# Kernel optimization log

Measured on AMD Instinct MI355X. Metric: run time of the kernel, lower is better.

Reference implementation:

```python
import jax, jax.numpy as jnp
import numpy as np

B, L, S, H, E = 2, 2048, 2048, 8, 64

def setup_inputs() -> dict:
    key = jax.random.key(0)
    k1, k2, k3 = jax.random.split(key, 3)
    queries = jax.random.normal(k1, (B, L, H, E), dtype=jnp.float32)
    keys = jax.random.normal(k2, (B, S, H, E), dtype=jnp.float32)
    values = jax.random.normal(k3, (B, S, H, E), dtype=jnp.float32)
    # TriangularCausalMask: True above the diagonal (positions to mask out)
    attn_mask = jnp.broadcast_to(
        jnp.triu(jnp.ones((L, S), dtype=bool), k=1)[None, None], (B, 1, L, S)
    )
    return {"queries": queries, "keys": keys, "values": values, "attn_mask": attn_mask}

def reference(queries, keys, values, attn_mask):
    E_ = queries.shape[-1]
    scale = 1.0 / (E_ ** 0.5)  # self.scale is None -> 1/sqrt(E)
    # scores: [B, H, L, S]
    scores = jnp.einsum('blhe,bshe->bhls', queries, keys)
    scores = jnp.where(attn_mask, -jnp.inf, scores)  # masked_fill_(mask, -inf)
    series = jax.nn.softmax(scale * scores, axis=-1)  # dropout p=0.0 -> identity
    V = jnp.einsum('bhls,bshd->blhd', series, values)
    return V, series
```

## Files before the change

### kernel.cpp

```cpp
#include <hip/hip_runtime.h>
#include <hip/hip_bf16.h>

typedef __attribute__((ext_vector_type(8))) short bf16x8;
typedef __attribute__((ext_vector_type(4))) short s16x4;
typedef __attribute__((ext_vector_type(4))) float f32x4;

constexpr int B = 2, L = 2048, S = 2048, H = 8, E = 64;
constexpr int TL = 64;
constexpr int SN = 64;
constexpr int LDK = 72;
constexpr int THREADS = 256;
constexpr int GSTR = H * E;

__device__ __forceinline__ short f2bf(float x) {
  union { float f; unsigned u; } c; c.f = x;
  unsigned r = c.u + 0x7fffu + ((c.u >> 16) & 1u);
  return (short)(r >> 16);
}
__device__ __forceinline__ float bf2f(short s) {
  union { unsigned u; float f; } c; c.u = ((unsigned)(unsigned short)s) << 16;
  return c.f;
}
__device__ __forceinline__ f32x4 mk4(float a, float b, float c, float d) {
  f32x4 v; v[0] = a; v[1] = b; v[2] = c; v[3] = d; return v;
}

struct Tile16 { f32x4 v0, v1, v2, v3; };

__device__ __forceinline__ void ld_tile(const float* __restrict__ g, int tid, Tile16& t) {
  const int r = tid >> 2, c = (tid & 3) * 16;
  const f32x4* q = (const f32x4*)(g + (size_t)r * GSTR + c);
  t.v0 = q[0]; t.v1 = q[1]; t.v2 = q[2]; t.v3 = q[3];
}

__device__ __forceinline__ void cvt_tile(const Tile16& t, short* __restrict__ o) {
  float vv[16] = { t.v0[0],t.v0[1],t.v0[2],t.v0[3], t.v1[0],t.v1[1],t.v1[2],t.v1[3],
                   t.v2[0],t.v2[1],t.v2[2],t.v2[3], t.v3[0],t.v3[1],t.v3[2],t.v3[3] };
#pragma unroll
  for (int k = 0; k < 8; ++k) {
    __hip_bfloat162 h = __float22bfloat162_rn(make_float2(vv[2*k], vv[2*k+1]));
    short2 s2 = *(short2*)&h;
    o[2*k] = s2.x; o[2*k+1] = s2.y;
  }
}

__device__ __forceinline__ void stK(const Tile16& t, short (* __restrict__ Kb)[LDK], int tid) {
  const int r = tid >> 2, c = (tid & 3) * 16;
  short s[16]; cvt_tile(t, s);
  *(bf16x8*)&Kb[r][c]     = *(bf16x8*)&s[0];
  *(bf16x8*)&Kb[r][c + 8] = *(bf16x8*)&s[8];
}

__device__ __forceinline__ void stV(const Tile16& t, short (* __restrict__ Vb)[LDK], int tid) {
  const int sr = tid >> 2, c = (tid & 3) * 16;
  short s[16]; cvt_tile(t, s);
#pragma unroll
  for (int i = 0; i < 16; ++i) {
    const int e = c + i;
    Vb[e][sr ^ (8 * ((e >> 3) & 7))] = s[i];
  }
}

__global__ __launch_bounds__(THREADS, 2)
void attn_tile(const float* __restrict__ Q, const float* __restrict__ K,
               const float* __restrict__ V, float* __restrict__ outV,
               float* __restrict__ outS)
{
  __shared__ __align__(16) short Qs[TL][LDK];
  __shared__ __align__(16) short Ks[2][SN][LDK];
  __shared__ __align__(16) short Vt[2][E][LDK];
  __shared__ __align__(16) short Ps[4][16][LDK];
  __shared__ float inv_lds[TL];

  const int tid  = threadIdx.x;
  const int lane = tid & 63;
  const int wv   = tid >> 6;
  const int quad = lane >> 4;
  const int n16  = lane & 15;

  int t = blockIdx.x;
  t = (t & 1) ? (31 - (t >> 1)) : (t >> 1);
  const int bh = blockIdx.y;
  const int b = bh >> 3, h = bh & 7;
  const int l0 = t * TL;
  const int s_hi = l0 + TL;
  const int nt = s_hi / SN;

  const size_t qbase = ((size_t)b * L * H + h) * E;
  const size_t kbase = ((size_t)b * S * H + h) * E;
  const size_t srow  = (size_t)bh * L * S;

  {
    const f32x4 z = {0.f, 0.f, 0.f, 0.f};
    for (int r = 0; r < TL; ++r) {
      f32x4* p = (f32x4*)(outS + srow + (size_t)(l0 + r) * S);
      for (int s4 = s_hi / 4 + tid; s4 < S / 4; s4 += THREADS)
        __builtin_nontemporal_store(z, p + s4);
    }
  }

  Tile16 pk;
  ld_tile(K + kbase, tid, pk);
  {
    Tile16 tq;
    ld_tile(Q + qbase + (size_t)l0 * GSTR, tid, tq);
    stK(tq, Qs, tid);
  }
  __syncthreads();

  bf16x8 a0 = *(const bf16x8*)&Qs[wv * 16 + n16][quad * 8];
  bf16x8 a1 = *(const bf16x8*)&Qs[wv * 16 + n16][32 + quad * 8];

  float rsum[4] = {0.f, 0.f, 0.f, 0.f};
  for (int st = 0; st < nt; ++st) {
    short (*Kb)[LDK] = Ks[st & 1];
    stK(pk, Kb, tid);
    if (st + 1 < nt)
      ld_tile(K + kbase + (size_t)(st + 1) * SN * GSTR, tid, pk);
    __syncthreads();

    const int s0 = st * SN;
#pragma unroll
    for (int nn = 0; nn < 4; ++nn) {
      bf16x8 b0 = *(const bf16x8*)&Kb[nn * 16 + n16][quad * 8];
      bf16x8 b1 = *(const bf16x8*)&Kb[nn * 16 + n16][32 + quad * 8];
      f32x4 acc = {0.f, 0.f, 0.f, 0.f};
      acc = __builtin_amdgcn_mfma_f32_16x16x32_bf16(a0, b0, acc, 0, 0, 0);
      acc = __builtin_amdgcn_mfma_f32_16x16x32_bf16(a1, b1, acc, 0, 0, 0);
#pragma unroll
      for (int r = 0; r < 4; ++r) {
        const int l = l0 + wv * 16 + quad * 4 + r;
        const int s = s0 + nn * 16 + n16;
        rsum[r] += (s <= l) ? __expf(acc[r] * 0.125f) : 0.f;
      }
    }
  }

  Tile16 pk2, pv2;
  ld_tile(K + kbase, tid, pk2);
  ld_tile(V + kbase, tid, pv2);

#pragma unroll
  for (int r = 0; r < 4; ++r)
#pragma unroll
    for (int off = 1; off < 16; off <<= 1)
      rsum[r] += __shfl_xor(rsum[r], off, 64);
  if (n16 == 0)
#pragma unroll
    for (int r = 0; r < 4; ++r)
      inv_lds[wv * 16 + quad * 4 + r] = 1.f / rsum[r];
  __syncthreads();

  float inv_r[4];
#pragma unroll
  for (int r = 0; r < 4; ++r) inv_r[r] = inv_lds[wv * 16 + quad * 4 + r];

  f32x4 oacc[4] = {{0,0,0,0},{0,0,0,0},{0,0,0,0},{0,0,0,0}};
  for (int st = 0; st < nt; ++st) {
    const int s0 = st * SN;
    short (*Kb)[LDK] = Ks[st & 1];
    short (*Vb)[LDK] = Vt[st & 1];
    stK(pk2, Kb, tid);
    stV(pv2, Vb, tid);
    if (st + 1 < nt) {
      ld_tile(K + kbase + (size_t)(st + 1) * SN * GSTR, tid, pk2);
      ld_tile(V + kbase + (size_t)(st + 1) * SN * GSTR, tid, pv2);
    }
    __syncthreads();

#pragma unroll
    for (int nn = 0; nn < 4; ++nn) {
      bf16x8 b0 = *(const bf16x8*)&Kb[nn * 16 + n16][quad * 8];
      bf16x8 b1 = *(const bf16x8*)&Kb[nn * 16 + n16][32 + quad * 8];
      f32x4 acc = {0.f, 0.f, 0.f, 0.f};
      acc = __builtin_amdgcn_mfma_f32_16x16x32_bf16(a0, b0, acc, 0, 0, 0);
      acc = __builtin_amdgcn_mfma_f32_16x16x32_bf16(a1, b1, acc, 0, 0, 0);
#pragma unroll
      for (int r = 0; r < 4; ++r) {
        const int l = l0 + wv * 16 + quad * 4 + r;
        const int s = s0 + nn * 16 + n16;
        float w = (s <= l) ? __expf(acc[r] * 0.125f) * inv_r[r] : 0.f;
        Ps[wv][quad * 4 + r][(nn * 16 + n16) ^ (8 * quad)] = f2bf(w);
      }
    }

    asm volatile("s_waitcnt lgkmcnt(0)" ::: "memory");

    {
      const int row = lane >> 2;
      const int sub = lane & 3;
      const int swz = 8 * (lane >> 4);
      float* dstrow = outS + srow + (size_t)(l0 + wv * 16 + row) * S + s0;
#pragma unroll
      for (int i = 0; i < 4; ++i) {
        const int c = (i * 16 + sub * 4) ^ swz;
        s16x4 pw = *(const s16x4*)&Ps[wv][row][c];
        f32x4 o = mk4(bf2f(pw[0]), bf2f(pw[1]), bf2f(pw[2]), bf2f(pw[3]));
        __builtin_nontemporal_store(o, (f32x4*)(dstrow + i * 16 + sub * 4));
      }
    }

    {
      const int psw = 8 * ((n16 >> 2) & 3);
      bf16x8 pa0 = *(const bf16x8*)&Ps[wv][n16][(quad * 8)      ^ psw];
      bf16x8 pa1 = *(const bf16x8*)&Ps[wv][n16][(32 + quad * 8) ^ psw];
#pragma unroll
      for (int nn = 0; nn < 4; ++nn) {
        const int e   = nn * 16 + n16;
        const int vsw = 8 * ((e >> 3) & 7);
        bf16x8 vb0 = *(const bf16x8*)&Vb[e][(quad * 8)      ^ vsw];
        bf16x8 vb1 = *(const bf16x8*)&Vb[e][(32 + quad * 8) ^ vsw];
        oacc[nn] = __builtin_amdgcn_mfma_f32_16x16x32_bf16(pa0, vb0, oacc[nn], 0, 0, 0);
        oacc[nn] = __builtin_amdgcn_mfma_f32_16x16x32_bf16(pa1, vb1, oacc[nn], 0, 0, 0);
      }
    }
  }

#pragma unroll
  for (int nn = 0; nn < 4; ++nn)
#pragma unroll
    for (int r = 0; r < 4; ++r) {
      const int l = l0 + wv * 16 + quad * 4 + r;
      __builtin_nontemporal_store(oacc[nn][r],
          &outV[qbase + (size_t)l * GSTR + nn * 16 + n16]);
    }
}

extern "C" void kernel_launch(void* const* d_in, const int* in_sizes, int n_in,
                              void* d_out, int out_size, void* d_ws, size_t ws_size,
                              hipStream_t stream) {
  const float* Q = (const float*)d_in[0];
  const float* K = (const float*)d_in[1];
  const float* V = (const float*)d_in[2];
  float* outV = (float*)d_out;
  float* outS = outV + (size_t)B * L * H * E;
  attn_tile<<<dim3(L / TL, B * H), THREADS, 0, stream>>>(Q, K, V, outV, outS);
}
```

Measured before the change: 408.4 us.

## Split attention into row-sum kernel and split-S PV kernel with atomics

Splits the single fused kernel into two launches. The first computes softmax denominators, zero-fills the masked score region and zeroes the output, writing inverse row sums to the workspace. The second splits each query tile's key range into two halves across separate blocks, accumulating output with atomicAdd. The aim is to give the heavy PV/score-write phase more parallelism and better load balance, at the cost of an extra launch, a global round-trip for the row sums, recomputed Q conversion, and atomic traffic.

After: 388.1 us. 1.05x faster.

```diff
diff --git a/kernel.cpp b/kernel.cpp
--- a/kernel.cpp
+++ b/kernel.cpp
@@ -12,14 +12,14 @@
 constexpr int THREADS = 256;
 constexpr int GSTR = H * E;
 
+__device__ __forceinline__ float bf2f(short s) {
+  union { unsigned u; float f; } c; c.u = ((unsigned)(unsigned short)s) << 16;
+  return c.f;
+}
 __device__ __forceinline__ short f2bf(float x) {
   union { float f; unsigned u; } c; c.f = x;
   unsigned r = c.u + 0x7fffu + ((c.u >> 16) & 1u);
   return (short)(r >> 16);
-}
-__device__ __forceinline__ float bf2f(short s) {
-  union { unsigned u; float f; } c; c.u = ((unsigned)(unsigned short)s) << 16;
-  return c.f;
 }
 __device__ __forceinline__ f32x4 mk4(float a, float b, float c, float d) {
   f32x4 v; v[0] = a; v[1] = b; v[2] = c; v[3] = d; return v;
@@ -61,16 +61,29 @@
   }
 }
 
+__device__ __forceinline__ bf16x8 cvt8(f32x4 u0, f32x4 u1) {
+  short o[8];
+  float vv[8] = { u0[0],u0[1],u0[2],u0[3], u1[0],u1[1],u1[2],u1[3] };
+#pragma unroll
+  for (int k = 0; k < 4; ++k) {
+    __hip_bfloat162 h = __float22bfloat162_rn(make_float2(vv[2*k], vv[2*k+1]));
+    short2 s2 = *(short2*)&h;
+    o[2*k] = s2.x; o[2*k+1] = s2.y;
+  }
+  return *(bf16x8*)o;
+}
+
+__device__ __forceinline__ int swz_t(int raw) {
+  return (raw & 1) ? (31 - (raw >> 1)) : (raw >> 1);
+}
+
 __global__ __launch_bounds__(THREADS, 2)
-void attn_tile(const float* __restrict__ Q, const float* __restrict__ K,
-               const float* __restrict__ V, float* __restrict__ outV,
-               float* __restrict__ outS)
+void k_rowsum(const float* __restrict__ Q, const float* __restrict__ K,
+              float* __restrict__ outV, float* __restrict__ outS,
+              float* __restrict__ ws)
 {
   __shared__ __align__(16) short Qs[TL][LDK];
   __shared__ __align__(16) short Ks[2][SN][LDK];
-  __shared__ __align__(16) short Vt[2][E][LDK];
-  __shared__ __align__(16) short Ps[4][16][LDK];
-  __shared__ float inv_lds[TL];
 
   const int tid  = threadIdx.x;
   const int lane = tid & 63;
@@ -78,8 +91,7 @@
   const int quad = lane >> 4;
   const int n16  = lane & 15;
 
-  int t = blockIdx.x;
-  t = (t & 1) ? (31 - (t >> 1)) : (t >> 1);
+  const int t  = swz_t(blockIdx.x);
   const int bh = blockIdx.y;
   const int b = bh >> 3, h = bh & 7;
   const int l0 = t * TL;
@@ -89,6 +101,16 @@
   const size_t qbase = ((size_t)b * L * H + h) * E;
   const size_t kbase = ((size_t)b * S * H + h) * E;
   const size_t srow  = (size_t)bh * L * S;
+
+  {
+    const f32x4 z = {0.f, 0.f, 0.f, 0.f};
+#pragma unroll
+    for (int i = 0; i < 4; ++i) {
+      const int idx = tid * 4 + i;
+      const int r = idx >> 4, c = idx & 15;
+      *(f32x4*)(outV + qbase + (size_t)(l0 + r) * GSTR + c * 4) = z;
+    }
+  }
 
   {
     const f32x4 z = {0.f, 0.f, 0.f, 0.f};
@@ -134,11 +156,8 @@
         rsum[r] += (s <= l) ? __expf(acc[r] * 0.125f) : 0.f;
       }
     }
-  }
-
-  Tile16 pk2, pv2;
-  ld_tile(K + kbase, tid, pk2);
-  ld_tile(V + kbase, tid, pv2);
+    __syncthreads();
+  }
 
 #pragma unroll
   for (int r = 0; r < 4; ++r)
@@ -148,21 +167,63 @@
   if (n16 == 0)
 #pragma unroll
     for (int r = 0; r < 4; ++r)
-      inv_lds[wv * 16 + quad * 4 + r] = 1.f / rsum[r];
-  __syncthreads();
+      ws[(size_t)bh * L + l0 + wv * 16 + quad * 4 + r] = 1.f / rsum[r];
+}
+
+__global__ __launch_bounds__(THREADS, 3)
+void k_pv(const float* __restrict__ Q, const float* __restrict__ K,
+          const float* __restrict__ V, float* __restrict__ outV,
+          float* __restrict__ outS, const float* __restrict__ ws)
+{
+  __shared__ __align__(16) short Ks[2][SN][LDK];
+  __shared__ __align__(16) short Vt[2][E][LDK];
+  __shared__ __align__(16) short Ps[4][16][LDK];
+
+  const int tid  = threadIdx.x;
+  const int lane = tid & 63;
+  const int wv   = tid >> 6;
+  const int quad = lane >> 4;
+  const int n16  = lane & 15;
+
+  const int t  = swz_t(blockIdx.x >> 1);
+  const int hh = blockIdx.x & 1;
+  const int bh = blockIdx.y;
+  const int b = bh >> 3, h = bh & 7;
+  const int l0 = t * TL;
+  const int nt = (l0 + TL) / SN;
+  const int st0 = hh ? (nt + 1) / 2 : 0;
+  const int st1 = hh ? nt : (nt + 1) / 2;
+
+  const size_t qbase = ((size_t)b * L * H + h) * E;
+  const size_t kbase = ((size_t)b * S * H + h) * E;
+  const size_t srow  = (size_t)bh * L * S;
+
+  const int qrow = l0 + wv * 16 + n16;
+  const float* qp = Q + qbase + (size_t)qrow * GSTR;
+  bf16x8 a0 = cvt8(*(const f32x4*)(qp + quad * 8), *(const f32x4*)(qp + quad * 8 + 4));
+  bf16x8 a1 = cvt8(*(const f32x4*)(qp + 32 + quad * 8), *(const f32x4*)(qp + 36 + quad * 8));
 
   float inv_r[4];
 #pragma unroll
-  for (int r = 0; r < 4; ++r) inv_r[r] = inv_lds[wv * 16 + quad * 4 + r];
+  for (int r = 0; r < 4; ++r)
+    inv_r[r] = ws[(size_t)bh * L + l0 + wv * 16 + quad * 4 + r];
 
   f32x4 oacc[4] = {{0,0,0,0},{0,0,0,0},{0,0,0,0},{0,0,0,0}};
-  for (int st = 0; st < nt; ++st) {
+
+  Tile16 pk2, pv2;
+  if (st0 < st1) {
+    ld_tile(K + kbase + (size_t)st0 * SN * GSTR, tid, pk2);
+    ld_tile(V + kbase + (size_t)st0 * SN * GSTR, tid, pv2);
+  }
+
+  for (int st = st0; st < st1; ++st) {
     const int s0 = st * SN;
-    short (*Kb)[LDK] = Ks[st & 1];
-    short (*Vb)[LDK] = Vt[st & 1];
+    const int buf = (st - st0) & 1;
+    short (*Kb)[LDK] = Ks[buf];
+    short (*Vb)[LDK] = Vt[buf];
     stK(pk2, Kb, tid);
     stV(pv2, Vb, tid);
-    if (st + 1 < nt) {
+    if (st + 1 < st1) {
       ld_tile(K + kbase + (size_t)(st + 1) * SN * GSTR, tid, pk2);
       ld_tile(V + kbase + (size_t)(st + 1) * SN * GSTR, tid, pv2);
     }
@@ -214,6 +275,7 @@
         oacc[nn] = __builtin_amdgcn_mfma_f32_16x16x32_bf16(pa1, vb1, oacc[nn], 0, 0, 0);
       }
     }
+    __syncthreads();
   }
 
 #pragma unroll
@@ -221,8 +283,7 @@
 #pragma unroll
     for (int r = 0; r < 4; ++r) {
       const int l = l0 + wv * 16 + quad * 4 + r;
-      __builtin_nontemporal_store(oacc[nn][r],
-          &outV[qbase + (size_t)l * GSTR + nn * 16 + n16]);
+      atomicAdd(&outV[qbase + (size_t)l * GSTR + nn * 16 + n16], oacc[nn][r]);
     }
 }
 
@@ -234,5 +295,7 @@
   const float* V = (const float*)d_in[2];
   float* outV = (float*)d_out;
   float* outS = outV + (size_t)B * L * H * E;
-  attn_tile<<<dim3(L / TL, B * H), THREADS, 0, stream>>>(Q, K, V, outV, outS);
-}
+  float* inv  = (float*)d_ws;
+  k_rowsum<<<dim3(L / TL, B * H), THREADS, 0, stream>>>(Q, K, outV, outS, inv);
+  k_pv<<<dim3(2 * L / TL, B * H), THREADS, 0, stream>>>(Q, K, V, outV, outS, inv);
+}
```
